# Kernel optimization log

Hardware: AMD Instinct MI355X
Metric: run time of the kernel (lower is better)

The kernel has to match this reference:

```python
import jax, jax.numpy as jnp
import numpy as np

B, H, W, C = 32, 64, 64, 512
NH, WH, WW = 16, 8, 8
SH, SW = 4, 4
FF = 2048
META = 384
A = WH * WW
EPS = 1e-5


def _rel_coords_log():
    # pairwise relative coords in log-space, shape (A*A, 2)
    coords = np.stack(np.meshgrid(np.arange(WH), np.arange(WW), indexing='ij')).reshape(2, -1)
    rel = coords[:, :, None] - coords[:, None, :]
    rel = rel.transpose(1, 2, 0).reshape(-1, 2).astype(np.float32)
    return np.sign(rel) * np.log1p(np.abs(rel))


def _attn_mask():
    # shifted-window attention mask, shape (nW, A, A)
    img = np.zeros((H, W), np.float32)
    cnt = 0
    for hs in (slice(0, -WH), slice(-WH, -SH), slice(-SH, None)):
        for ws in (slice(0, -WW), slice(-WW, -SW), slice(-SW, None)):
            img[hs, ws] = cnt
            cnt += 1
    mw = img.reshape(H // WH, WH, W // WW, WW).transpose(0, 2, 1, 3).reshape(-1, A)
    diff = mw[:, None, :] - mw[:, :, None]
    return np.where(diff != 0, -100.0, 0.0).astype(np.float32)


def setup_inputs():
    key = jax.random.key(0)
    ks = jax.random.split(key, 8)
    s = 0.02
    return {
        'x': jax.random.normal(ks[0], (B, H * W, C), jnp.float32),
        'qkv_w': jax.random.normal(ks[1], (C, 3 * C), jnp.float32) * s,
        'qkv_b': jnp.zeros((3 * C,), jnp.float32),
        'proj_w': jax.random.normal(ks[2], (C, C), jnp.float32) * s,
        'proj_b': jnp.zeros((C,), jnp.float32),
        'tau': jnp.ones((NH,), jnp.float32),
        'meta_w1': jax.random.normal(ks[3], (2, META), jnp.float32) * s,
        'meta_b1': jnp.zeros((META,), jnp.float32),
        'meta_w2': jax.random.normal(ks[4], (META, NH), jnp.float32) * s,
        'meta_b2': jnp.zeros((NH,), jnp.float32),
        'norm1_g': jnp.ones((C,), jnp.float32),
        'norm1_b': jnp.zeros((C,), jnp.float32),
        'norm2_g': jnp.ones((C,), jnp.float32),
        'norm2_b': jnp.zeros((C,), jnp.float32),
        'mlp_w1': jax.random.normal(ks[5], (C, FF), jnp.float32) * s,
        'mlp_b1': jnp.zeros((FF,), jnp.float32),
        'mlp_w2': jax.random.normal(ks[6], (FF, C), jnp.float32) * s,
        'mlp_b2': jnp.zeros((C,), jnp.float32),
    }


def _layernorm(x, g, b):
    mu = x.mean(-1, keepdims=True)
    var = ((x - mu) ** 2).mean(-1, keepdims=True)
    return (x - mu) * jax.lax.rsqrt(var + EPS) * g + b


def reference(x, qkv_w, qkv_b, proj_w, proj_b, tau, meta_w1, meta_b1, meta_w2, meta_b2,
              norm1_g, norm1_b, norm2_g, norm2_b, mlp_w1, mlp_b1, mlp_w2, mlp_b2):
    rel_log = jnp.asarray(_rel_coords_log())
    mask = jnp.asarray(_attn_mask())                 # (nW, A, A)
    nW = mask.shape[0]
    hd = C // NH

    # relative position bias from meta MLP (dropout inactive at eval)
    bias = jax.nn.relu(rel_log @ meta_w1 + meta_b1) @ meta_w2 + meta_b2  # (A*A, NH)
    bias = bias.T.reshape(NH, A, A)

    # cyclic shift + window partition
    xr = x.reshape(B, H, W, C)
    xr = jnp.roll(xr, (-SH, -SW), axis=(1, 2))
    xw = xr.reshape(B, H // WH, WH, W // WW, WW, C).transpose(0, 1, 3, 2, 4, 5)
    xw = xw.reshape(B * nW, A, C)

    qkv = (xw @ qkv_w + qkv_b).reshape(B * nW, A, 3, NH, hd).transpose(2, 0, 3, 1, 4)
    q, k, v = qkv[0], qkv[1], qkv[2]                 # (B*nW, NH, A, hd)

    qn = jnp.linalg.norm(q, axis=-1, keepdims=True)
    kn = jnp.linalg.norm(k, axis=-1, keepdims=True)
    denom = jnp.clip(qn * kn.transpose(0, 1, 3, 2), 1e-6, None)
    attn = jnp.einsum('wnid,wnjd->wnij', q, k) / denom
    attn = attn / jnp.clip(tau, 0.01, None).reshape(1, NH, 1, 1)
    attn = attn + bias[None]
    attn = attn.reshape(B, nW, NH, A, A) + mask[None, :, None]
    attn = jax.nn.softmax(attn.reshape(B * nW, NH, A, A), axis=-1)

    out = jnp.einsum('wnij,wnjd->wnid', attn, v)
    out = out.transpose(0, 2, 1, 3).reshape(B * nW, A, C)
    out = out @ proj_w + proj_b

    # window reverse + reverse shift
    out = out.reshape(B, H // WH, W // WW, WH, WW, C).transpose(0, 1, 3, 2, 4, 5).reshape(B, H, W, C)
    out = jnp.roll(out, (SH, SW), axis=(1, 2)).reshape(B, H * W, C)

    # swin-v2 post-norm residuals
    x = x + _layernorm(out, norm1_g, norm1_b)
    hmid = jax.nn.gelu(x @ mlp_w1 + mlp_b1, approximate=False) @ mlp_w2 + mlp_b2
    x = x + _layernorm(hmid, norm2_g, norm2_b)
    return x
```

## Files before the change

kernel.cpp:

```cpp
#include <hip/hip_runtime.h>

typedef unsigned short u16;
typedef __attribute__((ext_vector_type(8))) short     bf16x8;
typedef __attribute__((ext_vector_type(8))) unsigned short u16x8;
typedef __attribute__((ext_vector_type(4))) unsigned short u16x4;
typedef __attribute__((ext_vector_type(4))) float     f32x4;

#define GADDR(p) ((const __attribute__((address_space(1))) void*)(p))
#define LADDR(p) ((__attribute__((address_space(3))) void*)(p))

__device__ __forceinline__ u16 f2bf(float f) {
  unsigned u = __float_as_uint(f);
  u += 0x7fffu + ((u >> 16) & 1u);
  return (u16)(u >> 16);
}
__device__ __forceinline__ float bf2f(u16 h) {
  return __uint_as_float(((unsigned)h) << 16);
}

__global__ void wt_kernel(const float* __restrict__ w, u16* __restrict__ wt,
                          int K, int N) {
  size_t idx = (size_t)blockIdx.x * 256 + threadIdx.x;
  if (idx >= (size_t)K * N) return;
  int n = (int)(idx / K);
  int k = (int)(idx % K);
  wt[idx] = f2bf(w[(size_t)k * N + n]);
}

__global__ __launch_bounds__(64)
void bias_kernel(const float* __restrict__ w1, const float* __restrict__ b1,
                 const float* __restrict__ w2, const float* __restrict__ b2,
                 float* __restrict__ out) {
  const int p = blockIdx.x;
  const int i = p >> 6, j = p & 63;
  const float d0 = (float)((i >> 3) - (j >> 3));
  const float d1 = (float)((i & 7) - (j & 7));
  const float r0 = copysignf(log1pf(fabsf(d0)), d0);
  const float r1 = copysignf(log1pf(fabsf(d1)), d1);
  float part[16];
#pragma unroll
  for (int h = 0; h < 16; ++h) part[h] = 0.f;
  for (int m = threadIdx.x; m < 384; m += 64) {
    float hv = fmaxf(r0 * w1[m] + r1 * w1[384 + m] + b1[m], 0.f);
#pragma unroll
    for (int h = 0; h < 16; ++h) part[h] += hv * w2[m * 16 + h];
  }
#pragma unroll
  for (int h = 0; h < 16; ++h) {
    float v = part[h];
#pragma unroll
    for (int off = 32; off; off >>= 1) v += __shfl_xor(v, off);
    if (threadIdx.x == 0) out[(size_t)h * 4096 + p] = v + b2[h];
  }
}

__global__ __launch_bounds__(64)
void bias2_kernel(const float* __restrict__ bb, float* __restrict__ b2) {
  const int blk = blockIdx.x;
  const int h = blk >> 4, mi = (blk >> 2) & 3, ni = blk & 3;
  const int lane = threadIdx.x, fr = lane & 15, fq = lane >> 4;
  float4 o;
  o.x = bb[(size_t)h * 4096 + (mi * 16 + fq * 4 + 0) * 64 + ni * 16 + fr];
  o.y = bb[(size_t)h * 4096 + (mi * 16 + fq * 4 + 1) * 64 + ni * 16 + fr];
  o.z = bb[(size_t)h * 4096 + (mi * 16 + fq * 4 + 2) * 64 + ni * 16 + fr];
  o.w = bb[(size_t)h * 4096 + (mi * 16 + fq * 4 + 3) * 64 + ni * 16 + fr];
  ((float4*)b2)[(size_t)blk * 64 + lane] = o;
}

__global__ __launch_bounds__(128)
void partition_kernel(const float* __restrict__ x, u16* __restrict__ xw) {
  const size_t r = blockIdx.x;
  const int w   = (int)(r >> 6);
  const int i   = (int)(r & 63);
  const int b   = w >> 6;
  const int win = w & 63;
  const int hs = (((win >> 3) << 3) + (i >> 3) + 4) & 63;
  const int ws2 = (((win & 7) << 3) + (i & 7) + 4) & 63;
  const float4* src = (const float4*)(x + (((size_t)b << 12) + hs * 64 + ws2) * 512);
  u16* dst = xw + r * 512;
  const int t = threadIdx.x;
  float4 v = src[t];
  u16x4 o;
  o[0] = f2bf(v.x); o[1] = f2bf(v.y); o[2] = f2bf(v.z); o[3] = f2bf(v.w);
  *(u16x4*)(dst + t * 4) = o;
}

template <int MODE>
__global__ __launch_bounds__(512, 2)
void gemm8(const u16* __restrict__ A, const u16* __restrict__ Wt,
           const float* __restrict__ bias, void* __restrict__ outp,
           int M, int N, int K) {
  __shared__ u16 lds[4 * 16384];
  const int t = threadIdx.x;
  const int gx = gridDim.x;
  const int nwg = gx * gridDim.y;
  const int wg = blockIdx.y * gx + blockIdx.x;
  const int swz = (wg & 7) * (nwg >> 3) + (wg >> 3);
  const int n0 = (swz % gx) * 256;
  const int m0 = (swz / gx) * 256;

  const int lane = t & 63;
  const int wid = t >> 6;
  const int wr = (wid >> 2) * 128;
  const int wc = (wid & 3) * 64;
  const int fr = lane & 15, fq = lane >> 4;
  const int rx = (fr >> 1) & 3;

  const int srow = t >> 2;
  const int schk = ((t & 3) ^ ((srow >> 1) & 3)) * 8;
  const u16* Ag0 = A  + (size_t)(m0 + srow) * K + schk;
  const u16* Ag1 = Ag0 + (size_t)128 * K;
  const u16* Bg0 = Wt + (size_t)(n0 + srow) * K + schk;
  const u16* Bg1 = Bg0 + (size_t)128 * K;

#define STAGE(tile) do {                                                      \
    const int _o = ((tile) & 3) * 16384 + t * 8;                              \
    const size_t _k = (size_t)(tile) * 32;                                    \
    __builtin_amdgcn_global_load_lds(GADDR(Ag0 + _k), LADDR(&lds[_o]), 16, 0, 0); \
    __builtin_amdgcn_global_load_lds(GADDR(Ag1 + _k), LADDR(&lds[_o + 4096]), 16, 0, 0); \
    __builtin_amdgcn_global_load_lds(GADDR(Bg0 + _k), LADDR(&lds[_o + 8192]), 16, 0, 0); \
    __builtin_amdgcn_global_load_lds(GADDR(Bg1 + _k), LADDR(&lds[_o + 12288]), 16, 0, 0); \
  } while (0)

  f32x4 acc[8][4];
#pragma unroll
  for (int a = 0; a < 8; ++a)
#pragma unroll
    for (int b = 0; b < 4; ++b) acc[a][b] = (f32x4){0.f, 0.f, 0.f, 0.f};

  const int NT = K >> 5;
  STAGE(0); STAGE(1); STAGE(2);

  for (int u = 0; u < NT; ++u) {
    if (u + 2 < NT)      asm volatile("s_waitcnt vmcnt(8)" ::: "memory");
    else if (u + 1 < NT) asm volatile("s_waitcnt vmcnt(4)" ::: "memory");
    else                 asm volatile("s_waitcnt vmcnt(0)" ::: "memory");
    __builtin_amdgcn_s_barrier();

    const u16* lb = lds + (u & 3) * 16384;
    bf16x8 af[8], bfr[4];
#pragma unroll
    for (int mi = 0; mi < 8; ++mi)
      af[mi] = *(const bf16x8*)&lb[(wr + mi * 16 + fr) * 32 + (fq ^ rx) * 8];
#pragma unroll
    for (int ni = 0; ni < 4; ++ni)
      bfr[ni] = *(const bf16x8*)&lb[8192 + (wc + ni * 16 + fr) * 32 + (fq ^ rx) * 8];

    if (u + 3 < NT) STAGE(u + 3);

    __builtin_amdgcn_s_setprio(1);
#pragma unroll
    for (int mi = 0; mi < 8; ++mi)
#pragma unroll
      for (int ni = 0; ni < 4; ++ni)
        acc[mi][ni] = __builtin_amdgcn_mfma_f32_16x16x32_bf16(
            af[mi], bfr[ni], acc[mi][ni], 0, 0, 0);
    __builtin_amdgcn_s_setprio(0);
  }
#undef STAGE

  __syncthreads();
  float bv4[4];
#pragma unroll
  for (int ni = 0; ni < 4; ++ni) bv4[ni] = bias[n0 + wc + ni * 16 + fr];

  if (MODE == 1) {
    float* fW = (float*)&lds[wid * 8192];
    float* og = (float*)outp;
#pragma unroll
    for (int mi = 0; mi < 8; ++mi) {
#pragma unroll
      for (int ni = 0; ni < 4; ++ni)
#pragma unroll
        for (int j = 0; j < 4; ++j)
          fW[(fq * 4 + j) * 64 + ni * 16 + fr] = acc[mi][ni][j] + bv4[ni];
#pragma unroll
      for (int p = 0; p < 4; ++p) {
        f32x4 v = *(f32x4*)&fW[p * 256 + lane * 4];
        const int row = m0 + wr + mi * 16 + p * 4 + (lane >> 4);
        *(f32x4*)&og[(size_t)row * N + n0 + wc + (lane & 15) * 4] = v;
      }
    }
  } else {
    u16* uW = &lds[wid * 8192];
    u16* og = (u16*)outp;
#pragma unroll
    for (int mi = 0; mi < 8; ++mi) {
#pragma unroll
      for (int ni = 0; ni < 4; ++ni)
#pragma unroll
        for (int j = 0; j < 4; ++j) {
          float v = acc[mi][ni][j] + bv4[ni];
          if (MODE == 2) {
            const float a2 = v * (1.5957691216f + 0.0713548162f * v * v);
            const float e = __expf(a2);
            v = v * (e * __builtin_amdgcn_rcpf(e + 1.0f));
          }
          uW[(fq * 4 + j) * 64 + ni * 16 + fr] = f2bf(v);
        }
#pragma unroll
      for (int p = 0; p < 2; ++p) {
        u16x8 v8 = *(const u16x8*)&uW[p * 512 + lane * 8];
        const int row = m0 + wr + mi * 16 + p * 8 + (lane >> 3);
        *(u16x8*)&og[(size_t)row * N + n0 + wc + (lane & 7) * 8] = v8;
      }
    }
  }
}

__global__ __launch_bounds__(64)
void attn_kernel(const u16* __restrict__ qkv, const float* __restrict__ bias2,
                 const float* __restrict__ tau, u16* __restrict__ ao) {
  const int h = blockIdx.x;
  const int w = blockIdx.y;
  const int lane = threadIdx.x;
  const int fr = lane & 15, fq = lane >> 4;

  __shared__ u16 sh[7424];

  const size_t rowb = ((size_t)w * 64 + lane) * 1536 + (size_t)h * 32;
  u16x8 q8[4], k8[4], v8[4];
#pragma unroll
  for (int u = 0; u < 4; ++u) {
    q8[u] = ((const u16x8*)(qkv + rowb))[u];
    k8[u] = ((const u16x8*)(qkv + rowb + 512))[u];
    v8[u] = ((const u16x8*)(qkv + rowb + 1024))[u];
  }
  float qv[32], kv[32];
  float qn = 0.f, kn = 0.f;
#pragma unroll
  for (int d = 0; d < 32; ++d) {
    qv[d] = bf2f(q8[d >> 3][d & 7]); qn = fmaf(qv[d], qv[d], qn);
    kv[d] = bf2f(k8[d >> 3][d & 7]); kn = fmaf(kv[d], kv[d], kn);
  }
  const float itau = 1.0f / fmaxf(tau[h], 0.01f);
  const float qs = rsqrtf(fmaxf(qn, 1e-24f)) * itau;
  const float ks = rsqrtf(fmaxf(kn, 1e-24f));
#pragma unroll
  for (int u = 0; u < 4; ++u) {
    u16x8 qo, ko;
#pragma unroll
    for (int e = 0; e < 8; ++e) {
      qo[e] = f2bf(qv[u * 8 + e] * qs);
      ko[e] = f2bf(kv[u * 8 + e] * ks);
    }
    *(u16x8*)&sh[lane * 40 + u * 8] = qo;
    *(u16x8*)&sh[2560 + lane * 40 + u * 8] = ko;
  }
#pragma unroll
  for (int d = 0; d < 32; ++d)
    sh[5120 + d * 72 + lane] = v8[d >> 3][d & 7];
  __syncthreads();

  f32x4 acc[4][4];
  const float4* b2 = (const float4*)bias2 + (size_t)h * 1024 + lane;
#pragma unroll
  for (int mi = 0; mi < 4; ++mi)
#pragma unroll
    for (int ni = 0; ni < 4; ++ni) {
      float4 bv = b2[(mi * 4 + ni) * 64];
      acc[mi][ni] = (f32x4){bv.x, bv.y, bv.z, bv.w};
    }
  const int win = w & 63, wh = win >> 3, ww = win & 7;
  if (wh == 7 || ww == 7) {
    int labc[4];
#pragma unroll
    for (int ni = 0; ni < 4; ++ni) {
      const int c = ni * 16 + fr;
      labc[ni] = ((wh == 7) ? (((c >> 3) < 4) ? 1 : 2) : 0) * 3
               + ((ww == 7) ? (((c & 7) < 4) ? 1 : 2) : 0);
    }
#pragma unroll
    for (int mi = 0; mi < 4; ++mi)
#pragma unroll
      for (int j = 0; j < 4; ++j) {
        const int r = mi * 16 + fq * 4 + j;
        const int lr = ((wh == 7) ? (((r >> 3) < 4) ? 1 : 2) : 0) * 3
                     + ((ww == 7) ? (((r & 7) < 4) ? 1 : 2) : 0);
#pragma unroll
        for (int ni = 0; ni < 4; ++ni)
          if (lr != labc[ni]) acc[mi][ni][j] -= 100.f;
      }
  }

  {
    bf16x8 af[4], bf[4];
#pragma unroll
    for (int mi = 0; mi < 4; ++mi)
      af[mi] = *(const bf16x8*)&sh[(mi * 16 + fr) * 40 + fq * 8];
#pragma unroll
    for (int ni = 0; ni < 4; ++ni)
      bf[ni] = *(const bf16x8*)&sh[2560 + (ni * 16 + fr) * 40 + fq * 8];
#pragma unroll
    for (int mi = 0; mi < 4; ++mi)
#pragma unroll
      for (int ni = 0; ni < 4; ++ni)
        acc[mi][ni] = __builtin_amdgcn_mfma_f32_16x16x32_bf16(
            af[mi], bf[ni], acc[mi][ni], 0, 0, 0);
  }

  float lrec[4][4];
#pragma unroll
  for (int mi = 0; mi < 4; ++mi) {
#pragma unroll
    for (int j = 0; j < 4; ++j) {
      float m4 = fmaxf(fmaxf(acc[mi][0][j], acc[mi][1][j]),
                       fmaxf(acc[mi][2][j], acc[mi][3][j]));
#pragma unroll
      for (int mk = 1; mk < 16; mk <<= 1) m4 = fmaxf(m4, __shfl_xor(m4, mk));
      float e0 = __expf(acc[mi][0][j] - m4);
      float e1 = __expf(acc[mi][1][j] - m4);
      float e2 = __expf(acc[mi][2][j] - m4);
      float e3 = __expf(acc[mi][3][j] - m4);
      float s4 = (e0 + e1) + (e2 + e3);
#pragma unroll
      for (int mk = 1; mk < 16; mk <<= 1) s4 += __shfl_xor(s4, mk);
      lrec[mi][j] = __builtin_amdgcn_rcpf(s4);
      const int r = mi * 16 + fq * 4 + j;
      sh[r * 72 +  0 + fr] = f2bf(e0);
      sh[r * 72 + 16 + fr] = f2bf(e1);
      sh[r * 72 + 32 + fr] = f2bf(e2);
      sh[r * 72 + 48 + fr] = f2bf(e3);
    }
  }
  __syncthreads();

  f32x4 acc2[4][2];
#pragma unroll
  for (int mi = 0; mi < 4; ++mi)
#pragma unroll
    for (int n2 = 0; n2 < 2; ++n2) acc2[mi][n2] = (f32x4){0.f, 0.f, 0.f, 0.f};
#pragma unroll
  for (int kk = 0; kk < 2; ++kk) {
    bf16x8 pf[4], vf[2];
#pragma unroll
    for (int mi = 0; mi < 4; ++mi)
      pf[mi] = *(const bf16x8*)&sh[(mi * 16 + fr) * 72 + kk * 32 + fq * 8];
#pragma unroll
    for (int n2 = 0; n2 < 2; ++n2)
      vf[n2] = *(const bf16x8*)&sh[5120 + (n2 * 16 + fr) * 72 + kk * 32 + fq * 8];
#pragma unroll
    for (int mi = 0; mi < 4; ++mi)
#pragma unroll
      for (int n2 = 0; n2 < 2; ++n2)
        acc2[mi][n2] = __builtin_amdgcn_mfma_f32_16x16x32_bf16(
            pf[mi], vf[n2], acc2[mi][n2], 0, 0, 0);
  }

  u16* op = ao + ((size_t)w * 64) * 512 + (size_t)h * 32;
#pragma unroll
  for (int mi = 0; mi < 4; ++mi)
#pragma unroll
    for (int j = 0; j < 4; ++j) {
      const int r = mi * 16 + fq * 4 + j;
      const float sc = lrec[mi][j];
      op[(size_t)r * 512 +  0 + fr] = f2bf(acc2[mi][0][j] * sc);
      op[(size_t)r * 512 + 16 + fr] = f2bf(acc2[mi][1][j] * sc);
    }
}

__global__ __launch_bounds__(64)
void ln1_kernel(const float* __restrict__ pr, const float* __restrict__ x,
                const float* __restrict__ g, const float* __restrict__ bt,
                float* __restrict__ x1, u16* __restrict__ x1b) {
  const size_t tkn = blockIdx.x;
  const int b  = (int)(tkn >> 12);
  const int hh = (int)((tkn >> 6) & 63);
  const int ww = (int)(tkn & 63);
  const int hr = (hh - 4) & 63;
  const int wr = (ww - 4) & 63;
  const size_t prow = (((size_t)b * 64 + ((hr >> 3) << 3) + (wr >> 3)) * 64
                       + ((hr & 7) << 3) + (wr & 7)) * 512;
  const int l = threadIdx.x;
  float4 v0 = ((const float4*)(pr + prow))[2 * l];
  float4 v1 = ((const float4*)(pr + prow))[2 * l + 1];
  float s  = v0.x + v0.y + v0.z + v0.w + v1.x + v1.y + v1.z + v1.w;
  float s2 = v0.x*v0.x + v0.y*v0.y + v0.z*v0.z + v0.w*v0.w
           + v1.x*v1.x + v1.y*v1.y + v1.z*v1.z + v1.w*v1.w;
#pragma unroll
  for (int off = 32; off; off >>= 1) { s += __shfl_xor(s, off); s2 += __shfl_xor(s2, off); }
  const float mu = s * (1.f / 512.f);
  const float rs = rsqrtf(s2 * (1.f / 512.f) - mu * mu + 1e-5f);
  const int c0 = l * 8;
  const float* xp = x + tkn * 512 + c0;
  float vv[8] = {v0.x, v0.y, v0.z, v0.w, v1.x, v1.y, v1.z, v1.w};
  float* o = x1 + tkn * 512 + c0;
  u16x8 ob;
#pragma unroll
  for (int u = 0; u < 8; ++u) {
    float val = xp[u] + (vv[u] - mu) * rs * g[c0 + u] + bt[c0 + u];
    o[u] = val;
    ob[u] = f2bf(val);
  }
  *(u16x8*)(x1b + tkn * 512 + c0) = ob;
}

__global__ __launch_bounds__(64)
void ln2_kernel(float* __restrict__ io, const float* __restrict__ x1,
                const float* __restrict__ g, const float* __restrict__ bt) {
  const size_t tkn = blockIdx.x;
  const int l = threadIdx.x;
  float* row = io + tkn * 512;
  float4 v0 = ((const float4*)row)[2 * l];
  float4 v1 = ((const float4*)row)[2 * l + 1];
  float s  = v0.x + v0.y + v0.z + v0.w + v1.x + v1.y + v1.z + v1.w;
  float s2 = v0.x*v0.x + v0.y*v0.y + v0.z*v0.z + v0.w*v0.w
           + v1.x*v1.x + v1.y*v1.y + v1.z*v1.z + v1.w*v1.w;
#pragma unroll
  for (int off = 32; off; off >>= 1) { s += __shfl_xor(s, off); s2 += __shfl_xor(s2, off); }
  const float mu = s * (1.f / 512.f);
  const float rs = rsqrtf(s2 * (1.f / 512.f) - mu * mu + 1e-5f);
  const int c0 = l * 8;
  const float* xp = x1 + tkn * 512 + c0;
  float vv[8] = {v0.x, v0.y, v0.z, v0.w, v1.x, v1.y, v1.z, v1.w};
#pragma unroll
  for (int u = 0; u < 8; ++u)
    row[c0 + u] = xp[u] + (vv[u] - mu) * rs * g[c0 + u] + bt[c0 + u];
}

extern "C" void kernel_launch(void* const* d_in, const int* in_sizes, int n_in,
                              void* d_out, int out_size, void* d_ws, size_t ws_size,
                              hipStream_t stream) {
  const float* x      = (const float*)d_in[0];
  const float* qkv_w  = (const float*)d_in[1];
  const float* qkv_b  = (const float*)d_in[2];
  const float* proj_w = (const float*)d_in[3];
  const float* proj_b = (const float*)d_in[4];
  const float* tau    = (const float*)d_in[5];
  const float* mw1    = (const float*)d_in[6];
  const float* mb1    = (const float*)d_in[7];
  const float* mw2    = (const float*)d_in[8];
  const float* mb2    = (const float*)d_in[9];
  const float* n1g    = (const float*)d_in[10];
  const float* n1b    = (const float*)d_in[11];
  const float* n2g    = (const float*)d_in[12];
  const float* n2b    = (const float*)d_in[13];
  const float* mlp_w1 = (const float*)d_in[14];
  const float* mlp_b1 = (const float*)d_in[15];
  const float* mlp_w2 = (const float*)d_in[16];
  const float* mlp_b2 = (const float*)d_in[17];

  char* ws = (char*)d_ws;
  u16*   WQKVT  = (u16*)  (ws + 0);
  u16*   WPROJT = (u16*)  (ws + 1572864);
  u16*   WM1T   = (u16*)  (ws + 2097152);
  u16*   WM2T   = (u16*)  (ws + 4194304);
  float* BIASB  = (float*)(ws + 6291456);
  float* BIAS2  = (float*)(ws + 6553600);
  const size_t CH0 = 8388608;

  int CB = 32;
  while (CB > 1 && CH0 + (size_t)CB * 33554432ull > ws_size) CB >>= 1;
  const int NCH = 32 / CB;
  const size_t Mc = (size_t)CB * 4096;

  u16*   XW   = (u16*)  (ws + CH0);
  u16*   QKV  = (u16*)  (ws + CH0 + Mc * 1024);
  u16*   HBUF = QKV;
  float* X1   = (float*)(ws + CH0 + Mc * 5120);
  u16*   X1B  = (u16*)  (ws + CH0 + Mc * 7168);
  u16*   AO   = XW;

  wt_kernel<<<(512 * 1536 + 255) / 256, 256, 0, stream>>>(qkv_w, WQKVT, 512, 1536);
  wt_kernel<<<(512 * 512 + 255) / 256, 256, 0, stream>>>(proj_w, WPROJT, 512, 512);
  wt_kernel<<<(512 * 2048 + 255) / 256, 256, 0, stream>>>(mlp_w1, WM1T, 512, 2048);
  wt_kernel<<<(2048 * 512 + 255) / 256, 256, 0, stream>>>(mlp_w2, WM2T, 2048, 512);
  bias_kernel<<<4096, 64, 0, stream>>>(mw1, mb1, mw2, mb2, BIASB);
  bias2_kernel<<<256, 64, 0, stream>>>(BIASB, BIAS2);

  const unsigned MB = (unsigned)(Mc / 256);

  for (int c = 0; c < NCH; ++c) {
    const float* xc = x + (size_t)c * Mc * 512;
    float* oc = (float*)d_out + (size_t)c * Mc * 512;

    partition_kernel<<<(unsigned)Mc, 128, 0, stream>>>(xc, XW);
    gemm8<0><<<dim3(6, MB), 512, 0, stream>>>(XW, WQKVT, qkv_b, QKV,
                                              (int)Mc, 1536, 512);
    attn_kernel<<<dim3(16, CB * 64), 64, 0, stream>>>(QKV, BIAS2, tau, AO);
    gemm8<1><<<dim3(2, MB), 512, 0, stream>>>(AO, WPROJT, proj_b, oc,
                                              (int)Mc, 512, 512);
    ln1_kernel<<<(unsigned)Mc, 64, 0, stream>>>(oc, xc, n1g, n1b, X1, X1B);
    gemm8<2><<<dim3(8, MB), 512, 0, stream>>>(X1B, WM1T, mlp_b1, HBUF,
                                              (int)Mc, 2048, 512);
    gemm8<1><<<dim3(2, MB), 512, 0, stream>>>(HBUF, WM2T, mlp_b2, oc,
                                              (int)Mc, 512, 2048);
    ln2_kernel<<<(unsigned)Mc, 64, 0, stream>>>(oc, X1, n2g, n2b);
  }
}
```

Measured before the change: 1.656 ms.

## Fuse projection and MLP-down GEMMs with LayerNorm residual epilogues

Adds a gemm_ln kernel in which each workgroup computes full 128x512 output rows, so the bias, LayerNorm, residual add and window-reverse/unshift scatter run in the epilogue. This removes the separate ln1/ln2 kernels and the fp32 round trip of the projection and MLP outputs through global memory. The generic GEMM also interleaves its A/B staging loads with the LDS fragment reads, splits the MFMA loop into two halves, and uses a swizzled bf16 epilogue (its fp32 path is dropped). In exchange, the fused kernel launches only Mc/128 workgroups at one per CU with a 3-stage LDS ring, which may lower parallelism and latency hiding for the N=512 GEMMs.

```diff
diff --git a/kernel.cpp b/kernel.cpp
--- a/kernel.cpp
+++ b/kernel.cpp
@@ -113,11 +113,15 @@
   const u16* Bg0 = Wt + (size_t)(n0 + srow) * K + schk;
   const u16* Bg1 = Bg0 + (size_t)128 * K;
 
-#define STAGE(tile) do {                                                      \
+#define STAGE_A(tile) do {                                                    \
     const int _o = ((tile) & 3) * 16384 + t * 8;                              \
     const size_t _k = (size_t)(tile) * 32;                                    \
     __builtin_amdgcn_global_load_lds(GADDR(Ag0 + _k), LADDR(&lds[_o]), 16, 0, 0); \
     __builtin_amdgcn_global_load_lds(GADDR(Ag1 + _k), LADDR(&lds[_o + 4096]), 16, 0, 0); \
+  } while (0)
+#define STAGE_B(tile) do {                                                    \
+    const int _o = ((tile) & 3) * 16384 + t * 8;                              \
+    const size_t _k = (size_t)(tile) * 32;                                    \
     __builtin_amdgcn_global_load_lds(GADDR(Bg0 + _k), LADDR(&lds[_o + 8192]), 16, 0, 0); \
     __builtin_amdgcn_global_load_lds(GADDR(Bg1 + _k), LADDR(&lds[_o + 12288]), 16, 0, 0); \
   } while (0)
@@ -129,7 +133,7 @@
     for (int b = 0; b < 4; ++b) acc[a][b] = (f32x4){0.f, 0.f, 0.f, 0.f};
 
   const int NT = K >> 5;
-  STAGE(0); STAGE(1); STAGE(2);
+  STAGE_A(0); STAGE_B(0); STAGE_A(1); STAGE_B(1); STAGE_A(2); STAGE_B(2);
 
   for (int u = 0; u < NT; ++u) {
     if (u + 2 < NT)      asm volatile("s_waitcnt vmcnt(8)" ::: "memory");
@@ -138,73 +142,230 @@
     __builtin_amdgcn_s_barrier();
 
     const u16* lb = lds + (u & 3) * 16384;
-    bf16x8 af[8], bfr[4];
-#pragma unroll
-    for (int mi = 0; mi < 8; ++mi)
-      af[mi] = *(const bf16x8*)&lb[(wr + mi * 16 + fr) * 32 + (fq ^ rx) * 8];
+    bf16x8 bfr[4], af0[4], af1[4];
 #pragma unroll
     for (int ni = 0; ni < 4; ++ni)
       bfr[ni] = *(const bf16x8*)&lb[8192 + (wc + ni * 16 + fr) * 32 + (fq ^ rx) * 8];
-
-    if (u + 3 < NT) STAGE(u + 3);
+#pragma unroll
+    for (int mi = 0; mi < 4; ++mi)
+      af0[mi] = *(const bf16x8*)&lb[(wr + mi * 16 + fr) * 32 + (fq ^ rx) * 8];
+    if (u + 3 < NT) STAGE_A(u + 3);
+#pragma unroll
+    for (int mi = 0; mi < 4; ++mi)
+      af1[mi] = *(const bf16x8*)&lb[(wr + 64 + mi * 16 + fr) * 32 + (fq ^ rx) * 8];
+    if (u + 3 < NT) STAGE_B(u + 3);
 
     __builtin_amdgcn_s_setprio(1);
 #pragma unroll
-    for (int mi = 0; mi < 8; ++mi)
+    for (int mi = 0; mi < 4; ++mi)
 #pragma unroll
       for (int ni = 0; ni < 4; ++ni)
         acc[mi][ni] = __builtin_amdgcn_mfma_f32_16x16x32_bf16(
-            af[mi], bfr[ni], acc[mi][ni], 0, 0, 0);
+            af0[mi], bfr[ni], acc[mi][ni], 0, 0, 0);
     __builtin_amdgcn_s_setprio(0);
-  }
-#undef STAGE
+    __builtin_amdgcn_s_setprio(1);
+#pragma unroll
+    for (int mi = 0; mi < 4; ++mi)
+#pragma unroll
+      for (int ni = 0; ni < 4; ++ni)
+        acc[4 + mi][ni] = __builtin_amdgcn_mfma_f32_16x16x32_bf16(
+            af1[mi], bfr[ni], acc[4 + mi][ni], 0, 0, 0);
+    __builtin_amdgcn_s_setprio(0);
+  }
+#undef STAGE_A
+#undef STAGE_B
 
   __syncthreads();
   float bv4[4];
 #pragma unroll
   for (int ni = 0; ni < 4; ++ni) bv4[ni] = bias[n0 + wc + ni * 16 + fr];
 
-  if (MODE == 1) {
-    float* fW = (float*)&lds[wid * 8192];
-    float* og = (float*)outp;
-#pragma unroll
-    for (int mi = 0; mi < 8; ++mi) {
+  u16* uW = &lds[wid * 8192];
+  u16* og = (u16*)outp;
+#pragma unroll
+  for (int mi = 0; mi < 8; ++mi) {
+#pragma unroll
+    for (int ni = 0; ni < 4; ++ni)
+#pragma unroll
+      for (int j = 0; j < 4; ++j) {
+        float v = acc[mi][ni][j] + bv4[ni];
+        if (MODE == 2) {
+          const float a2 = v * (1.5957691216f + 0.0713548162f * v * v);
+          const float e = __expf(a2);
+          v = v * (e * __builtin_amdgcn_rcpf(e + 1.0f));
+        }
+        uW[(fq * 4 + j) * 64 + ((ni ^ j ^ fq) & 3) * 16 + fr] = f2bf(v);
+      }
+#pragma unroll
+    for (int p = 0; p < 2; ++p) {
+      const int r = p * 8 + (lane >> 3);
+      const int sg = (((lane & 7) >> 1) ^ (r & 3) ^ ((r >> 2) & 3)) & 3;
+      u16x8 v8 = *(const u16x8*)&uW[r * 64 + sg * 16 + (lane & 1) * 8];
+      const int row = m0 + wr + mi * 16 + r;
+      *(u16x8*)&og[(size_t)row * N + n0 + wc + (lane & 7) * 8] = v8;
+    }
+  }
+}
+
+template <int LNM>
+__global__ __launch_bounds__(512, 1)
+void gemm_ln(const u16* __restrict__ A, const u16* __restrict__ Wt,
+             const float* __restrict__ bias, const float* __restrict__ resid,
+             const float* __restrict__ g, const float* __restrict__ bt,
+             float* __restrict__ out1, u16* __restrict__ out1b, int K) {
+  __shared__ u16 lds[61440];
+  const int t = threadIdx.x;
+  const int nwg = gridDim.x;
+  const int wg = blockIdx.x;
+  const int swz = (wg & 7) * (nwg >> 3) + (wg >> 3);
+  const int m0 = swz * 128;
+
+  const int lane = t & 63;
+  const int wid = t >> 6;
+  const int wc = wid * 64;
+  const int fr = lane & 15, fq = lane >> 4;
+  const int rx = (fr >> 1) & 3;
+
+  const int srow = t >> 2;
+  const int schk = ((t & 3) ^ ((srow >> 1) & 3)) * 8;
+  const u16* Ag = A  + (size_t)(m0 + srow) * K + schk;
+  const u16* Bg = Wt + (size_t)srow * K + schk;
+
+#define GLSTAGE_A(tile, buf)                                                  \
+    __builtin_amdgcn_global_load_lds(GADDR(Ag + (size_t)(tile) * 32),         \
+        LADDR(&lds[(buf) * 20480 + t * 8]), 16, 0, 0)
+#define GLSTAGE_B(tile, buf, p)                                               \
+    __builtin_amdgcn_global_load_lds(                                         \
+        GADDR(Bg + (size_t)(p) * 128 * K + (size_t)(tile) * 32),              \
+        LADDR(&lds[(buf) * 20480 + 4096 + (p) * 4096 + t * 8]), 16, 0, 0)
+
+  f32x4 acc[8][4];
+#pragma unroll
+  for (int a = 0; a < 8; ++a)
+#pragma unroll
+    for (int b = 0; b < 4; ++b) acc[a][b] = (f32x4){0.f, 0.f, 0.f, 0.f};
+
+  const int NT = K >> 5;
+  GLSTAGE_A(0, 0);
+  GLSTAGE_B(0, 0, 0); GLSTAGE_B(0, 0, 1); GLSTAGE_B(0, 0, 2); GLSTAGE_B(0, 0, 3);
+  GLSTAGE_A(1, 1);
+  GLSTAGE_B(1, 1, 0); GLSTAGE_B(1, 1, 1); GLSTAGE_B(1, 1, 2); GLSTAGE_B(1, 1, 3);
+
+  int cur = 0;
+  for (int u = 0; u < NT; ++u) {
+    if (u + 1 < NT) asm volatile("s_waitcnt vmcnt(5)" ::: "memory");
+    else            asm volatile("s_waitcnt vmcnt(0)" ::: "memory");
+    __builtin_amdgcn_s_barrier();
+
+    const u16* lb = lds + cur * 20480;
+    const int stg = (cur == 0) ? 2 : cur - 1;
+    bf16x8 bfr[4], af0[4], af1[4];
+#pragma unroll
+    for (int ni = 0; ni < 4; ++ni)
+      bfr[ni] = *(const bf16x8*)&lb[4096 + (wc + ni * 16 + fr) * 32 + (fq ^ rx) * 8];
+#pragma unroll
+    for (int mi = 0; mi < 4; ++mi)
+      af0[mi] = *(const bf16x8*)&lb[(mi * 16 + fr) * 32 + (fq ^ rx) * 8];
+    if (u + 2 < NT) {
+      GLSTAGE_A(u + 2, stg);
+      GLSTAGE_B(u + 2, stg, 0); GLSTAGE_B(u + 2, stg, 1);
+    }
+#pragma unroll
+    for (int mi = 0; mi < 4; ++mi)
+      af1[mi] = *(const bf16x8*)&lb[((4 + mi) * 16 + fr) * 32 + (fq ^ rx) * 8];
+    if (u + 2 < NT) {
+      GLSTAGE_B(u + 2, stg, 2); GLSTAGE_B(u + 2, stg, 3);
+    }
+
+    __builtin_amdgcn_s_setprio(1);
+#pragma unroll
+    for (int mi = 0; mi < 4; ++mi)
 #pragma unroll
       for (int ni = 0; ni < 4; ++ni)
-#pragma unroll
-        for (int j = 0; j < 4; ++j)
-          fW[(fq * 4 + j) * 64 + ni * 16 + fr] = acc[mi][ni][j] + bv4[ni];
-#pragma unroll
-      for (int p = 0; p < 4; ++p) {
-        f32x4 v = *(f32x4*)&fW[p * 256 + lane * 4];
-        const int row = m0 + wr + mi * 16 + p * 4 + (lane >> 4);
-        *(f32x4*)&og[(size_t)row * N + n0 + wc + (lane & 15) * 4] = v;
+        acc[mi][ni] = __builtin_amdgcn_mfma_f32_16x16x32_bf16(
+            af0[mi], bfr[ni], acc[mi][ni], 0, 0, 0);
+    __builtin_amdgcn_s_setprio(0);
+    __builtin_amdgcn_s_setprio(1);
+#pragma unroll
+    for (int mi = 0; mi < 4; ++mi)
+#pragma unroll
+      for (int ni = 0; ni < 4; ++ni)
+        acc[4 + mi][ni] = __builtin_amdgcn_mfma_f32_16x16x32_bf16(
+            af1[mi], bfr[ni], acc[4 + mi][ni], 0, 0, 0);
+    __builtin_amdgcn_s_setprio(0);
+    cur = (cur == 2) ? 0 : cur + 1;
+  }
+#undef GLSTAGE_A
+#undef GLSTAGE_B
+
+  __syncthreads();
+  float bv4[4];
+#pragma unroll
+  for (int ni = 0; ni < 4; ++ni) bv4[ni] = bias[wc + ni * 16 + fr];
+  float4 ga = ((const float4*)g)[lane * 2];
+  float4 gb = ((const float4*)g)[lane * 2 + 1];
+  float4 ba = ((const float4*)bt)[lane * 2];
+  float4 bb = ((const float4*)bt)[lane * 2 + 1];
+  const float gv[8] = {ga.x, ga.y, ga.z, ga.w, gb.x, gb.y, gb.z, gb.w};
+  const float bv[8] = {ba.x, ba.y, ba.z, ba.w, bb.x, bb.y, bb.z, bb.w};
+  float* fLN = (float*)lds;
+
+#pragma unroll
+  for (int mi = 0; mi < 8; ++mi) {
+#pragma unroll
+    for (int ni = 0; ni < 4; ++ni)
+#pragma unroll
+      for (int j = 0; j < 4; ++j) {
+        const int ch = ((wid * 4 + ni) ^ (j << 2) ^ fq) & 31;
+        fLN[(fq * 4 + j) * 512 + ch * 16 + fr] = acc[mi][ni][j] + bv4[ni];
       }
-    }
-  } else {
-    u16* uW = &lds[wid * 8192];
-    u16* og = (u16*)outp;
-#pragma unroll
-    for (int mi = 0; mi < 8; ++mi) {
-#pragma unroll
-      for (int ni = 0; ni < 4; ++ni)
-#pragma unroll
-        for (int j = 0; j < 4; ++j) {
-          float v = acc[mi][ni][j] + bv4[ni];
-          if (MODE == 2) {
-            const float a2 = v * (1.5957691216f + 0.0713548162f * v * v);
-            const float e = __expf(a2);
-            v = v * (e * __builtin_amdgcn_rcpf(e + 1.0f));
-          }
-          uW[(fq * 4 + j) * 64 + ni * 16 + fr] = f2bf(v);
-        }
-#pragma unroll
-      for (int p = 0; p < 2; ++p) {
-        u16x8 v8 = *(const u16x8*)&uW[p * 512 + lane * 8];
-        const int row = m0 + wr + mi * 16 + p * 8 + (lane >> 3);
-        *(u16x8*)&og[(size_t)row * N + n0 + wc + (lane & 7) * 8] = v8;
+    __syncthreads();
+#pragma unroll
+    for (int rr = 0; rr < 2; ++rr) {
+      const int r = wid * 2 + rr;
+      const int gci = lane >> 1;
+      const int ch = (gci ^ ((r & 3) << 2) ^ (r >> 2)) & 31;
+      const int base = r * 512 + ch * 16 + (lane & 1) * 8;
+      f32x4 va = *(const f32x4*)&fLN[base];
+      f32x4 vb = *(const f32x4*)&fLN[base + 4];
+      float v[8] = {va[0], va[1], va[2], va[3], vb[0], vb[1], vb[2], vb[3]};
+      float s = 0.f, s2 = 0.f;
+#pragma unroll
+      for (int e = 0; e < 8; ++e) { s += v[e]; s2 = fmaf(v[e], v[e], s2); }
+#pragma unroll
+      for (int off = 32; off; off >>= 1) {
+        s += __shfl_xor(s, off); s2 += __shfl_xor(s2, off);
       }
-    }
+      const float mu = s * (1.f / 512.f);
+      const float rs = rsqrtf(s2 * (1.f / 512.f) - mu * mu + 1e-5f);
+      const int rowg = m0 + mi * 16 + r;
+      size_t token;
+      if (LNM == 0) {
+        const int w = rowg >> 6, i = rowg & 63;
+        const int b = w >> 6, win = w & 63;
+        const int hs = (((win >> 3) << 3) + (i >> 3) + 4) & 63;
+        const int ws2 = (((win & 7) << 3) + (i & 7) + 4) & 63;
+        token = ((size_t)b << 12) + hs * 64 + ws2;
+      } else {
+        token = (size_t)rowg;
+      }
+      const float* rp = resid + token * 512 + lane * 8;
+      float4 r0 = ((const float4*)rp)[0];
+      float4 r1 = ((const float4*)rp)[1];
+      const float rv[8] = {r0.x, r0.y, r0.z, r0.w, r1.x, r1.y, r1.z, r1.w};
+      float o[8];
+      u16x8 ob;
+#pragma unroll
+      for (int e = 0; e < 8; ++e) {
+        o[e] = rv[e] + (v[e] - mu) * rs * gv[e] + bv[e];
+        ob[e] = f2bf(o[e]);
+      }
+      float* op = out1 + token * 512 + lane * 8;
+      ((f32x4*)op)[0] = (f32x4){o[0], o[1], o[2], o[3]};
+      ((f32x4*)op)[1] = (f32x4){o[4], o[5], o[6], o[7]};
+      if (LNM == 0) *(u16x8*)(out1b + token * 512 + lane * 8) = ob;
+    }
+    __syncthreads();
   }
 }
 
@@ -357,65 +518,6 @@
       op[(size_t)r * 512 +  0 + fr] = f2bf(acc2[mi][0][j] * sc);
       op[(size_t)r * 512 + 16 + fr] = f2bf(acc2[mi][1][j] * sc);
     }
-}
-
-__global__ __launch_bounds__(64)
-void ln1_kernel(const float* __restrict__ pr, const float* __restrict__ x,
-                const float* __restrict__ g, const float* __restrict__ bt,
-                float* __restrict__ x1, u16* __restrict__ x1b) {
-  const size_t tkn = blockIdx.x;
-  const int b  = (int)(tkn >> 12);
-  const int hh = (int)((tkn >> 6) & 63);
-  const int ww = (int)(tkn & 63);
-  const int hr = (hh - 4) & 63;
-  const int wr = (ww - 4) & 63;
-  const size_t prow = (((size_t)b * 64 + ((hr >> 3) << 3) + (wr >> 3)) * 64
-                       + ((hr & 7) << 3) + (wr & 7)) * 512;
-  const int l = threadIdx.x;
-  float4 v0 = ((const float4*)(pr + prow))[2 * l];
-  float4 v1 = ((const float4*)(pr + prow))[2 * l + 1];
-  float s  = v0.x + v0.y + v0.z + v0.w + v1.x + v1.y + v1.z + v1.w;
-  float s2 = v0.x*v0.x + v0.y*v0.y + v0.z*v0.z + v0.w*v0.w
-           + v1.x*v1.x + v1.y*v1.y + v1.z*v1.z + v1.w*v1.w;
-#pragma unroll
-  for (int off = 32; off; off >>= 1) { s += __shfl_xor(s, off); s2 += __shfl_xor(s2, off); }
-  const float mu = s * (1.f / 512.f);
-  const float rs = rsqrtf(s2 * (1.f / 512.f) - mu * mu + 1e-5f);
-  const int c0 = l * 8;
-  const float* xp = x + tkn * 512 + c0;
-  float vv[8] = {v0.x, v0.y, v0.z, v0.w, v1.x, v1.y, v1.z, v1.w};
-  float* o = x1 + tkn * 512 + c0;
-  u16x8 ob;
-#pragma unroll
-  for (int u = 0; u < 8; ++u) {
-    float val = xp[u] + (vv[u] - mu) * rs * g[c0 + u] + bt[c0 + u];
-    o[u] = val;
-    ob[u] = f2bf(val);
-  }
-  *(u16x8*)(x1b + tkn * 512 + c0) = ob;
-}
-
-__global__ __launch_bounds__(64)
-void ln2_kernel(float* __restrict__ io, const float* __restrict__ x1,
-                const float* __restrict__ g, const float* __restrict__ bt) {
-  const size_t tkn = blockIdx.x;
-  const int l = threadIdx.x;
-  float* row = io + tkn * 512;
-  float4 v0 = ((const float4*)row)[2 * l];
-  float4 v1 = ((const float4*)row)[2 * l + 1];
-  float s  = v0.x + v0.y + v0.z + v0.w + v1.x + v1.y + v1.z + v1.w;
-  float s2 = v0.x*v0.x + v0.y*v0.y + v0.z*v0.z + v0.w*v0.w
-           + v1.x*v1.x + v1.y*v1.y + v1.z*v1.z + v1.w*v1.w;
-#pragma unroll
-  for (int off = 32; off; off >>= 1) { s += __shfl_xor(s, off); s2 += __shfl_xor(s2, off); }
-  const float mu = s * (1.f / 512.f);
-  const float rs = rsqrtf(s2 * (1.f / 512.f) - mu * mu + 1e-5f);
-  const int c0 = l * 8;
-  const float* xp = x1 + tkn * 512 + c0;
-  float vv[8] = {v0.x, v0.y, v0.z, v0.w, v1.x, v1.y, v1.z, v1.w};
-#pragma unroll
-  for (int u = 0; u < 8; ++u)
-    row[c0 + u] = xp[u] + (vv[u] - mu) * rs * g[c0 + u] + bt[c0 + u];
 }
 
 extern "C" void kernel_launch(void* const* d_in, const int* in_sizes, int n_in,
@@ -469,6 +571,7 @@
   bias2_kernel<<<256, 64, 0, stream>>>(BIASB, BIAS2);
 
   const unsigned MB = (unsigned)(Mc / 256);
+  const unsigned LB = (unsigned)(Mc / 128);
 
   for (int c = 0; c < NCH; ++c) {
     const float* xc = x + (size_t)c * Mc * 512;
@@ -478,13 +581,11 @@
     gemm8<0><<<dim3(6, MB), 512, 0, stream>>>(XW, WQKVT, qkv_b, QKV,
                                               (int)Mc, 1536, 512);
     attn_kernel<<<dim3(16, CB * 64), 64, 0, stream>>>(QKV, BIAS2, tau, AO);
-    gemm8<1><<<dim3(2, MB), 512, 0, stream>>>(AO, WPROJT, proj_b, oc,
-                                              (int)Mc, 512, 512);
-    ln1_kernel<<<(unsigned)Mc, 64, 0, stream>>>(oc, xc, n1g, n1b, X1, X1B);
+    gemm_ln<0><<<LB, 512, 0, stream>>>(AO, WPROJT, proj_b, xc, n1g, n1b,
+                                       X1, X1B, 512);
     gemm8<2><<<dim3(8, MB), 512, 0, stream>>>(X1B, WM1T, mlp_b1, HBUF,
                                               (int)Mc, 2048, 512);
-    gemm8<1><<<dim3(2, MB), 512, 0, stream>>>(HBUF, WM2T, mlp_b2, oc,
-                                              (int)Mc, 512, 2048);
-    ln2_kernel<<<(unsigned)Mc, 64, 0, stream>>>(oc, X1, n2g, n2b);
-  }
-}
+    gemm_ln<1><<<LB, 512, 0, stream>>>(HBUF, WM2T, mlp_b2, X1, n2g, n2b,
+                                       oc, nullptr, 2048);
+  }
+}
```

Result: faster. 1.532 ms (-7.5%).
